# Kernel tuning notes

Measured on AMD Instinct MI355X. Metric: run time of the kernel, lower is better.

## Reference

```python
import jax, jax.numpy as jnp
import numpy as np

EPS = 1e-08
STEPS_START = 0
STEPS_END = 500


def setup_inputs() -> dict:
    key = jax.random.key(0)
    k_x, k_w, k_beta, k_b = jax.random.split(key, 4)
    B, T, D_in, D_out = 64, 500, 1024, 128
    x = jax.random.normal(k_x, (B, T, D_in), dtype=jnp.float32)
    # w ~ N(w_init_mean, w_init_std * sqrt(1/input_shape))
    w = jax.random.normal(k_w, (D_in, D_out), dtype=jnp.float32) * np.sqrt(1.0 / D_in)
    beta = jax.random.uniform(k_beta, (D_out,), dtype=jnp.float32)  # clamped to [0,1] in torch
    b = jax.random.uniform(k_b, (D_out,), dtype=jnp.float32)        # clamped >= 0 in torch
    return {"x": x, "w": w, "beta": beta, "b": b}


def reference(x, w, beta, b):
    # x: [B, T, D_in], w: [D_in, D_out], beta/b: [D_out]
    h = jnp.einsum('btc,cd->btd', x, w)          # [B, T, D_out]
    norm = jnp.sum(w * w, axis=0)                # [D_out]

    one_minus_beta = 1.0 - beta

    def step(mem, h_t):
        mem = mem * beta + one_minus_beta * h_t  # Leaky_Neuron=True
        return mem, mem

    mem0 = jnp.zeros((x.shape[0], w.shape[1]), dtype=x.dtype)
    _, mem_rec = jax.lax.scan(step, mem0, jnp.swapaxes(h, 0, 1))  # [T, B, D_out]
    mem_rec = jnp.swapaxes(mem_rec, 0, 1)                          # [B, T, D_out]

    # time_reduction == 'mean'
    output = jnp.mean(mem_rec[:, STEPS_START:STEPS_END, :], axis=1) / (norm + EPS) - b
    return output
```

## Files before the change

### kernel.cpp

```cpp
#include <hip/hip_runtime.h>
#include <hip/hip_bf16.h>

#define B_    64
#define T_    500
#define DIN   1024
#define DOUT  128
#define EPSV  1e-8f
#define BM    128
#define NKC   4
#define KCL   (DIN / NKC)
#define NST   (KCL / 32)
#define TILES 4
#define NGEMM (B_ * TILES * NKC)
#define NPREP 32
#define BCOLB 528

typedef __attribute__((ext_vector_type(8))) short bf16x8;
typedef __attribute__((ext_vector_type(4))) float f32x4;

#define OFF_NORM  262144
#define OFF_PART  278528

__device__ inline short f2bf(float f) {
    __hip_bfloat16 h = __float2bfloat16(f);
    return __builtin_bit_cast(short, h);
}

__global__ __launch_bounds__(512) void prep_kernel(
    const float* __restrict__ w, __hip_bfloat16* __restrict__ wT,
    float* __restrict__ normPart)
{
    const int tid = threadIdx.x;
    const int blk = blockIdx.x;
    const int t   = blk * 512 + tid;
    const int d   = t & 127;
    const int kq  = t >> 7;
    float v[8];
    float ss = 0.f;
#pragma unroll
    for (int m = 0; m < 8; ++m) {
        v[m] = w[(size_t)(kq * 8 + m) * DOUT + d];
        ss += v[m] * v[m];
    }
    bf16x8 o;
#pragma unroll
    for (int m = 0; m < 8; ++m) o[m] = f2bf(v[m]);
    *reinterpret_cast<bf16x8*>(wT + (size_t)d * DIN + kq * 8) = o;

    __shared__ float red[512];
    red[tid] = ss;
    __syncthreads();
    if (tid < 128)
        normPart[blk * DOUT + tid] = red[tid] + red[tid + 128] + red[tid + 256] + red[tid + 384];
}

__global__ __launch_bounds__(512, 4) void gemm_kernel(
    const float* __restrict__ x, const float* __restrict__ beta,
    const __hip_bfloat16* __restrict__ wT, float* __restrict__ partials)
{
    __shared__ __align__(16) char bsh[DOUT * BCOLB];
    __shared__ float red[8][DOUT];

    const int tid  = threadIdx.x;
    const int wid  = tid >> 6;
    const int lane = tid & 63;
    const int arow = lane & 15;
    const int kblk = lane >> 4;

    const int wg   = blockIdx.x;
    const int kc   = wg & 3;
    const int tile = (wg >> 2) & 3;
    const int b    = wg >> 4;
    const int t0   = tile * BM;
    const int kbase = kc * KCL;

    {
        const int col = tid >> 2;
        const int c4  = tid & 3;
        const __hip_bfloat16* src = wT + (size_t)col * DIN + kbase;
#pragma unroll
        for (int j = 0; j < 8; ++j) {
            int e = c4 * 8 + j * 32;
            bf16x8 v = *reinterpret_cast<const bf16x8*>(src + e);
            *reinterpret_cast<bf16x8*>(bsh + col * BCOLB + e * 2) = v;
        }
    }
    __syncthreads();

    const int trow_raw = t0 + wid * 16 + arow;
    const int trow = trow_raw < T_ ? trow_raw : T_ - 1;
    const float* ax = x + ((size_t)b * T_ + trow) * DIN + kbase + kblk * 8;

    int bro[8];
#pragma unroll
    for (int fn = 0; fn < 8; ++fn)
        bro[fn] = (fn * 16 + arow) * BCOLB + kblk * 16;

    f32x4 acc[8] = {};

    float4 a0 = *reinterpret_cast<const float4*>(ax);
    float4 a1 = *reinterpret_cast<const float4*>(ax + 4);
#pragma unroll
    for (int s = 0; s < NST; ++s) {
        float4 n0, n1;
        if (s + 1 < NST) {
            n0 = *reinterpret_cast<const float4*>(ax + (s + 1) * 32);
            n1 = *reinterpret_cast<const float4*>(ax + (s + 1) * 32 + 4);
        }
        bf16x8 af;
        af[0] = f2bf(a0.x); af[1] = f2bf(a0.y); af[2] = f2bf(a0.z); af[3] = f2bf(a0.w);
        af[4] = f2bf(a1.x); af[5] = f2bf(a1.y); af[6] = f2bf(a1.z); af[7] = f2bf(a1.w);
#pragma unroll
        for (int fn = 0; fn < 8; ++fn) {
            bf16x8 bf = *reinterpret_cast<const bf16x8*>(bsh + bro[fn] + s * 64);
            acc[fn] = __builtin_amdgcn_mfma_f32_16x16x32_bf16(af, bf, acc[fn], 0, 0, 0);
        }
        if (s + 1 < NST) { a0 = n0; a1 = n1; }
    }

#pragma unroll
    for (int fn = 0; fn < 8; ++fn) {
        const int col = fn * 16 + arow;
        const float lb = log2f(beta[col]);
        float s = 0.f;
#pragma unroll
        for (int r = 0; r < 4; ++r) {
            int t = t0 + wid * 16 + kblk * 4 + r;
            if (t < T_)
                s += (1.f - exp2f((float)(T_ - t) * lb)) * acc[fn][r];
        }
        s += __shfl_xor(s, 16);
        s += __shfl_xor(s, 32);
        if (kblk == 0) red[wid][col] = s;
    }
    __syncthreads();

    if (tid < DOUT) {
        float v = 0.f;
#pragma unroll
        for (int ww = 0; ww < 8; ++ww) v += red[ww][tid];
        partials[(((size_t)b * TILES + tile) * NKC + kc) * DOUT + tid] = v;
    }
}

__global__ __launch_bounds__(256) void finalize_kernel(
    const float* __restrict__ partials, const float* __restrict__ normPart,
    const float* __restrict__ bias, float* __restrict__ out)
{
    int i = blockIdx.x * 256 + threadIdx.x;
    int b = i >> 7, d = i & 127;
    float nrm = 0.f;
#pragma unroll
    for (int g = 0; g < NPREP; ++g)
        nrm += normPart[g * DOUT + d];
    float scale = 1.f / ((nrm + EPSV) * (float)T_);
    float s = 0.f;
#pragma unroll
    for (int p = 0; p < TILES * NKC; ++p)
        s += partials[((size_t)b * TILES * NKC + p) * DOUT + d];
    out[i] = s * scale - bias[d];
}

extern "C" void kernel_launch(void* const* d_in, const int* in_sizes, int n_in,
                              void* d_out, int out_size, void* d_ws, size_t ws_size,
                              hipStream_t stream) {
    const float* x    = (const float*)d_in[0];
    const float* w    = (const float*)d_in[1];
    const float* beta = (const float*)d_in[2];
    const float* bias = (const float*)d_in[3];
    float* out = (float*)d_out;

    char* ws = (char*)d_ws;
    __hip_bfloat16* wT = (__hip_bfloat16*)(ws);
    float* normPart = (float*)(ws + OFF_NORM);
    float* partials = (float*)(ws + OFF_PART);

    prep_kernel<<<NPREP, 512, 0, stream>>>(w, wT, normPart);
    gemm_kernel<<<NGEMM, 512, 0, stream>>>(x, beta, wT, partials);
    finalize_kernel<<<(B_ * DOUT) / 256, 256, 0, stream>>>(partials, normPart, bias, out);
}
```

Before: 41.94 us.

## Restructure GEMM into double-buffered LDS K-tiles with 2x2 warp tiling

Replaces the design that preloads the whole B slice into LDS and streams A directly from global memory into registers. The new kernel uses 64-row tiles, 256-thread blocks and a 2x2 wave layout, and stages both A (converted to bf16) and B through double-buffered, XOR-swizzled LDS tiles, with register prefetch two K-steps ahead. This is meant to raise operand reuse per wave and overlap global loads with MFMA work. In exchange it adds a barrier per K-step and doubles the number of blocks and partial sums, which adds finalize traffic.

After: 41.18 us. About the same (-1.8%).

```diff
diff --git a/kernel.cpp b/kernel.cpp
--- a/kernel.cpp
+++ b/kernel.cpp
@@ -6,14 +6,14 @@
 #define DIN   1024
 #define DOUT  128
 #define EPSV  1e-8f
-#define BM    128
+#define BM    64
+#define BK    32
 #define NKC   4
 #define KCL   (DIN / NKC)
-#define NST   (KCL / 32)
-#define TILES 4
+#define NKT   (KCL / BK)
+#define TILES 8
 #define NGEMM (B_ * TILES * NKC)
 #define NPREP 32
-#define BCOLB 528
 
 typedef __attribute__((ext_vector_type(8))) short bf16x8;
 typedef __attribute__((ext_vector_type(4))) float f32x4;
@@ -24,6 +24,12 @@
 __device__ inline short f2bf(float f) {
     __hip_bfloat16 h = __float2bfloat16(f);
     return __builtin_bit_cast(short, h);
+}
+
+__device__ inline void block_sync_lds() {
+    asm volatile("s_waitcnt lgkmcnt(0)" ::: "memory");
+    __builtin_amdgcn_s_barrier();
+    asm volatile("" ::: "memory");
 }
 
 __global__ __launch_bounds__(512) void prep_kernel(
@@ -54,91 +60,130 @@
         normPart[blk * DOUT + tid] = red[tid] + red[tid + 128] + red[tid + 256] + red[tid + 384];
 }
 
-__global__ __launch_bounds__(512, 4) void gemm_kernel(
+__global__ __launch_bounds__(256, 4) void gemm_kernel(
     const float* __restrict__ x, const float* __restrict__ beta,
     const __hip_bfloat16* __restrict__ wT, float* __restrict__ partials)
 {
-    __shared__ __align__(16) char bsh[DOUT * BCOLB];
-    __shared__ float red[8][DOUT];
+    __shared__ __align__(16) char smem[2 * 12288];
+    __shared__ float red[2][DOUT];
 
     const int tid  = threadIdx.x;
     const int wid  = tid >> 6;
     const int lane = tid & 63;
     const int arow = lane & 15;
     const int kblk = lane >> 4;
+    const int wr   = wid >> 1;
+    const int wc   = wid & 1;
 
     const int wg   = blockIdx.x;
     const int kc   = wg & 3;
-    const int tile = (wg >> 2) & 3;
-    const int b    = wg >> 4;
+    const int tile = (wg >> 2) & 7;
+    const int b    = wg >> 5;
     const int t0   = tile * BM;
     const int kbase = kc * KCL;
 
-    {
-        const int col = tid >> 2;
-        const int c4  = tid & 3;
-        const __hip_bfloat16* src = wT + (size_t)col * DIN + kbase;
-#pragma unroll
-        for (int j = 0; j < 8; ++j) {
-            int e = c4 * 8 + j * 32;
-            bf16x8 v = *reinterpret_cast<const bf16x8*>(src + e);
-            *reinterpret_cast<bf16x8*>(bsh + col * BCOLB + e * 2) = v;
+    const int srow = tid >> 2;
+    const int c4   = tid & 3;
+    int trow = t0 + srow; if (trow >= T_) trow = T_ - 1;
+    const float* ag = x + ((size_t)b * T_ + trow) * DIN + kbase + c4 * 8;
+    const int awoff = srow * 64 + ((c4 ^ (srow & 3)) << 4);
+    const int bcol = tid >> 1;
+    const int sh   = (tid & 1) * 2;
+    const __hip_bfloat16* bg = wT + (size_t)bcol * DIN + kbase + sh * 8;
+    const int bwoff0 = bcol * 64 + (((sh)     ^ (bcol & 3)) << 4);
+    const int bwoff1 = bcol * 64 + (((sh + 1) ^ (bcol & 3)) << 4);
+
+    int aro[2], bro[4];
+#pragma unroll
+    for (int fm = 0; fm < 2; ++fm) {
+        int row = wr * 32 + fm * 16 + arow;
+        aro[fm] = row * 64 + ((kblk ^ (row & 3)) << 4);
+    }
+#pragma unroll
+    for (int fn = 0; fn < 4; ++fn) {
+        int col = wc * 64 + fn * 16 + arow;
+        bro[fn] = col * 64 + ((kblk ^ (col & 3)) << 4);
+    }
+
+    f32x4 acc[2][4] = {};
+
+#define DECL_SET(S) float4 S##a0, S##a1; bf16x8 S##b0, S##b1;
+#define LOAD_SET(S, KB) \
+    S##a0 = *reinterpret_cast<const float4*>(ag + (KB));      \
+    S##a1 = *reinterpret_cast<const float4*>(ag + (KB) + 4);  \
+    S##b0 = *reinterpret_cast<const bf16x8*>(bg + (KB));      \
+    S##b1 = *reinterpret_cast<const bf16x8*>(bg + (KB) + 8);
+#define WRITE_SET(S, AB, BB) { \
+    bf16x8 ha; \
+    ha[0]=f2bf(S##a0.x); ha[1]=f2bf(S##a0.y); ha[2]=f2bf(S##a0.z); ha[3]=f2bf(S##a0.w); \
+    ha[4]=f2bf(S##a1.x); ha[5]=f2bf(S##a1.y); ha[6]=f2bf(S##a1.z); ha[7]=f2bf(S##a1.w); \
+    *reinterpret_cast<bf16x8*>((AB) + awoff)  = ha;      \
+    *reinterpret_cast<bf16x8*>((BB) + bwoff0) = S##b0;   \
+    *reinterpret_cast<bf16x8*>((BB) + bwoff1) = S##b1; }
+#define COMPUTE(AB, BB) { \
+    bf16x8 af0 = *reinterpret_cast<const bf16x8*>((AB) + aro[0]); \
+    bf16x8 af1 = *reinterpret_cast<const bf16x8*>((AB) + aro[1]); \
+    _Pragma("unroll") \
+    for (int fn = 0; fn < 4; ++fn) { \
+        bf16x8 bf = *reinterpret_cast<const bf16x8*>((BB) + bro[fn]); \
+        acc[0][fn] = __builtin_amdgcn_mfma_f32_16x16x32_bf16(af0, bf, acc[0][fn], 0, 0, 0); \
+        acc[1][fn] = __builtin_amdgcn_mfma_f32_16x16x32_bf16(af1, bf, acc[1][fn], 0, 0, 0); \
+    } }
+
+    DECL_SET(qe_) DECL_SET(qo_)
+
+    LOAD_SET(qe_, 0)
+    LOAD_SET(qo_, BK)
+    WRITE_SET(qe_, smem, smem + 4096)
+    block_sync_lds();
+
+#pragma unroll
+    for (int kt = 0; kt < NKT; ++kt) {
+        char* Acur = smem + (kt & 1) * 12288;
+        char* Bcur = Acur + 4096;
+        char* Anxt = smem + ((kt + 1) & 1) * 12288;
+        char* Bnxt = Anxt + 4096;
+
+        if (kt + 2 < NKT) {
+            if (kt & 1) { LOAD_SET(qo_, (kt + 2) * BK) }
+            else        { LOAD_SET(qe_, (kt + 2) * BK) }
         }
-    }
-    __syncthreads();
-
-    const int trow_raw = t0 + wid * 16 + arow;
-    const int trow = trow_raw < T_ ? trow_raw : T_ - 1;
-    const float* ax = x + ((size_t)b * T_ + trow) * DIN + kbase + kblk * 8;
-
-    int bro[8];
-#pragma unroll
-    for (int fn = 0; fn < 8; ++fn)
-        bro[fn] = (fn * 16 + arow) * BCOLB + kblk * 16;
-
-    f32x4 acc[8] = {};
-
-    float4 a0 = *reinterpret_cast<const float4*>(ax);
-    float4 a1 = *reinterpret_cast<const float4*>(ax + 4);
-#pragma unroll
-    for (int s = 0; s < NST; ++s) {
-        float4 n0, n1;
-        if (s + 1 < NST) {
-            n0 = *reinterpret_cast<const float4*>(ax + (s + 1) * 32);
-            n1 = *reinterpret_cast<const float4*>(ax + (s + 1) * 32 + 4);
+
+        COMPUTE(Acur, Bcur)
+
+        if (kt + 1 < NKT) {
+            if (kt & 1) { WRITE_SET(qe_, Anxt, Bnxt) }
+            else        { WRITE_SET(qo_, Anxt, Bnxt) }
+            block_sync_lds();
         }
-        bf16x8 af;
-        af[0] = f2bf(a0.x); af[1] = f2bf(a0.y); af[2] = f2bf(a0.z); af[3] = f2bf(a0.w);
-        af[4] = f2bf(a1.x); af[5] = f2bf(a1.y); af[6] = f2bf(a1.z); af[7] = f2bf(a1.w);
-#pragma unroll
-        for (int fn = 0; fn < 8; ++fn) {
-            bf16x8 bf = *reinterpret_cast<const bf16x8*>(bsh + bro[fn] + s * 64);
-            acc[fn] = __builtin_amdgcn_mfma_f32_16x16x32_bf16(af, bf, acc[fn], 0, 0, 0);
-        }
-        if (s + 1 < NST) { a0 = n0; a1 = n1; }
-    }
-
-#pragma unroll
-    for (int fn = 0; fn < 8; ++fn) {
-        const int col = fn * 16 + arow;
+    }
+#undef DECL_SET
+#undef LOAD_SET
+#undef WRITE_SET
+#undef COMPUTE
+
+#pragma unroll
+    for (int fn = 0; fn < 4; ++fn) {
+        const int col = wc * 64 + fn * 16 + arow;
         const float lb = log2f(beta[col]);
         float s = 0.f;
 #pragma unroll
-        for (int r = 0; r < 4; ++r) {
-            int t = t0 + wid * 16 + kblk * 4 + r;
-            if (t < T_)
-                s += (1.f - exp2f((float)(T_ - t) * lb)) * acc[fn][r];
+        for (int fm = 0; fm < 2; ++fm) {
+#pragma unroll
+            for (int r = 0; r < 4; ++r) {
+                int t = t0 + wr * 32 + fm * 16 + kblk * 4 + r;
+                if (t < T_)
+                    s += (1.f - exp2f((float)(T_ - t) * lb)) * acc[fm][fn][r];
+            }
         }
         s += __shfl_xor(s, 16);
         s += __shfl_xor(s, 32);
-        if (kblk == 0) red[wid][col] = s;
+        if (kblk == 0) red[wr][col] = s;
     }
     __syncthreads();
 
     if (tid < DOUT) {
-        float v = 0.f;
-#pragma unroll
-        for (int ww = 0; ww < 8; ++ww) v += red[ww][tid];
+        float v = red[0][tid] + red[1][tid];
         partials[(((size_t)b * TILES + tile) * NKC + kc) * DOUT + tid] = v;
     }
 }
@@ -176,6 +221,6 @@
     float* partials = (float*)(ws + OFF_PART);
 
     prep_kernel<<<NPREP, 512, 0, stream>>>(w, wT, normPart);
-    gemm_kernel<<<NGEMM, 512, 0, stream>>>(x, beta, wT, partials);
+    gemm_kernel<<<NGEMM, 256, 0, stream>>>(x, beta, wT, partials);
     finalize_kernel<<<(B_ * DOUT) / 256, 256, 0, stream>>>(partials, normPart, bias, out);
 }
```
